# Optimization experiments

Measured on AMD Instinct MI355X. Metric: run time of the kernel, lower is better.

Reference implementation:

```python
import jax, jax.numpy as jnp
import numpy as np

B, T, W, D = 4, 1000, 32, 200
ED, N, DCONV, DTR = 400, 16, 4, 13  # d_inner=2*d_model, d_state, d_conv, dt_rank=ceil(200/16)


def _causal_conv(x, w, b):
    # x: (B, L, ED), depthwise causal conv, kernel DCONV
    L = x.shape[1]
    xp = jnp.pad(x, ((0, 0), (DCONV - 1, 0), (0, 0)))
    y = sum(xp[:, k:k + L, :] * w[:, k] for k in range(DCONV))
    return y + b


def _ssm(x, A_log, Dp, xproj, dtw, dtb):
    # selective scan; x: (B, L, ED)
    A = -jnp.exp(A_log)                      # (ED, N)
    dbc = x @ xproj                          # (B, L, DTR+2N)
    delta, Bm, Cm = dbc[..., :DTR], dbc[..., DTR:DTR + N], dbc[..., DTR + N:]
    dt = jax.nn.softplus(delta @ dtw + dtb)  # (B, L, ED)
    dA = jnp.exp(dt[..., None] * A)                         # (B, L, ED, N)
    dBx = dt[..., None] * Bm[:, :, None, :] * x[..., None]  # (B, L, ED, N)

    def step(h, t):
        dA_t, dBx_t, C_t = t
        h = dA_t * h + dBx_t
        y = jnp.einsum('ben,bn->be', h, C_t)
        return h, y

    h0 = jnp.zeros((x.shape[0], ED, N), x.dtype)
    xs = (dA.transpose(1, 0, 2, 3), dBx.transpose(1, 0, 2, 3), Cm.transpose(1, 0, 2))
    _, ys = jax.lax.scan(step, h0, xs)
    return ys.transpose(1, 0, 2) + Dp * x


def _branch(x, in_proj, conv_w, conv_b, xproj, dtw, dtb, A_log, Dp):
    xz = x @ in_proj
    xp, z = xz[..., :ED], xz[..., ED:]
    xp = jax.nn.silu(_causal_conv(xp, conv_w, conv_b))
    y = _ssm(xp, A_log, Dp, xproj, dtw, dtb)
    return y * jax.nn.silu(z)


def setup_inputs() -> dict:
    key = jax.random.key(0)
    ks = jax.random.split(key, 24)
    s = 0.02
    nrm = lambda k, shape: jax.random.normal(k, shape, jnp.float32) * s
    inp = {}
    inp['input_ids'] = jax.random.normal(ks[0], (B, T, W, D), jnp.float32)
    inp['n_tweets'] = jax.random.randint(ks[1], (B,), 1, T + 1)
    inp['n_words'] = jax.random.randint(ks[2], (B, T), 1, W + 1)
    inp['cls_token'] = jnp.zeros((1, 1, D), jnp.float32)
    inp['w_attn'] = nrm(ks[3], (D, 1))
    inp['b_attn'] = jnp.zeros((1,), jnp.float32)
    inp['norm_w'] = jnp.ones((D,), jnp.float32)
    for i, d in enumerate(('f', 'b')):
        o = i * 8
        inp[f'in_proj_{d}'] = nrm(ks[4 + o], (D, 2 * ED))
        inp[f'conv_w_{d}'] = nrm(ks[5 + o], (ED, DCONV))
        inp[f'conv_b_{d}'] = jnp.zeros((ED,), jnp.float32)
        inp[f'xproj_{d}'] = nrm(ks[6 + o], (ED, DTR + 2 * N))
        inp[f'dtw_{d}'] = nrm(ks[7 + o], (DTR, ED))
        inp[f'dtb_{d}'] = jnp.zeros((ED,), jnp.float32)
        inp[f'A_log_{d}'] = jnp.log(jnp.broadcast_to(jnp.arange(1, N + 1, dtype=jnp.float32), (ED, N)))
        inp[f'D_{d}'] = jnp.ones((ED,), jnp.float32)
    inp['out_proj'] = nrm(ks[20], (ED, D))
    inp['head_w'] = nrm(ks[21], (D, 1))
    inp['head_b'] = jnp.zeros((1,), jnp.float32)
    return inp


def reference(input_ids, n_tweets, n_words, cls_token, w_attn, b_attn, norm_w,
              in_proj_f, conv_w_f, conv_b_f, xproj_f, dtw_f, dtb_f, A_log_f, D_f,
              in_proj_b, conv_w_b, conv_b_b, xproj_b, dtw_b, dtb_b, A_log_b, D_b,
              out_proj, head_w, head_b):
    Bz, Tz, Wz, Dz = input_ids.shape
    # ragged per-tweet attention pooling, fully vectorized with masks
    scores = jnp.squeeze(input_ids @ w_attn, -1) + b_attn[0]        # (B, T, W)
    wmask = jnp.arange(Wz) < n_words[..., None]                     # (B, T, W)
    scores = jnp.where(wmask, scores, -jnp.inf)
    attn = jax.nn.softmax(scores, axis=-1)
    tw = jnp.einsum('btw,btwd->btd', attn, input_ids)               # (B, T, D)
    tmask = jnp.arange(Tz) < n_tweets[:, None]
    tw = jnp.where(tmask[..., None], tw, 0.0)                       # padded tweets stay zero
    pos = Tz // 2
    x = jnp.concatenate([tw[:, :pos], jnp.broadcast_to(cls_token, (Bz, 1, Dz)), tw[:, pos:]], axis=1)
    # one bidirectional Mamba layer: pre-RMSNorm residual block
    xn = x * jax.lax.rsqrt(jnp.mean(x * x, axis=-1, keepdims=True) + 1e-5) * norm_w
    y_f = _branch(xn, in_proj_f, conv_w_f, conv_b_f, xproj_f, dtw_f, dtb_f, A_log_f, D_f)
    y_b = jnp.flip(_branch(jnp.flip(xn, 1), in_proj_b, conv_w_b, conv_b_b, xproj_b, dtw_b, dtb_b, A_log_b, D_b), 1)
    x = x + (y_f + y_b) @ out_proj
    logit = jnp.squeeze(x[:, pos] @ head_w, -1) + head_b[0]
    return jax.nn.sigmoid(logit)
```

## Files before the change

kernel.cpp:

```cpp
#include <hip/hip_runtime.h>
#include <cmath>

#define Bz 4
#define Tz 1000
#define Wz 32
#define Dz 200
#define EDz 400
#define Nz 16
#define DTRz 13
#define Lz 1001
#define POSz 500
#define LPz 501
#define TSTR 512
#define ESP 10
#define NEG_BIG -1e30f

__device__ __forceinline__ float wave_sum(float v) {
#pragma unroll
  for (int o = 32; o; o >>= 1) v += __shfl_xor(v, o);
  return v;
}

__global__ __launch_bounds__(256) void k_front(
    const float* __restrict__ x, const int* __restrict__ n_tweets,
    const int* __restrict__ n_words, const float* __restrict__ w_attn,
    const float* __restrict__ b_attn, const float* __restrict__ norm_w,
    const float* __restrict__ cls, const float* __restrict__ out_proj,
    const float* __restrict__ head_w, const float* __restrict__ ipf,
    const float* __restrict__ ipb, float* __restrict__ xn,
    float* __restrict__ zbuf, float* __restrict__ vbuf) {
  int bid = blockIdx.x;
  int tid = threadIdx.x;
  int wave = tid >> 6, lane = tid & 63;
  if (bid < 9) {
    if (bid == 0) {
      __shared__ float hw[Dz];
      if (tid < Dz) hw[tid] = head_w[tid];
      __syncthreads();
      for (int e = tid; e < EDz; e += 256) {
        float acc = 0.f;
        for (int d = 0; d < Dz; d += 4) {
          float4 ov = *(const float4*)(out_proj + e * Dz + d);
          acc += ov.x * hw[d] + ov.y * hw[d + 1] + ov.z * hw[d + 2] + ov.w * hw[d + 3];
        }
        vbuf[e] = acc;
      }
      return;
    }
    int id = bid - 1;
    int br = id >> 2, b = id & 3;
    __shared__ float xs[Dz];
    __shared__ float s_red[4];
    float val = (tid < Dz) ? cls[tid] : 0.f;
    float sq = wave_sum(val * val);
    if ((tid & 63) == 0) s_red[tid >> 6] = sq;
    __syncthreads();
    float tot = s_red[0] + s_red[1] + s_red[2] + s_red[3];
    float scale = rsqrtf(tot * (1.f / Dz) + 1e-5f);
    if (tid < Dz) {
      float o = val * scale * norm_w[tid];
      xs[tid] = o;
      if (br == 0) xn[((size_t)b * Lz + POSz) * Dz + tid] = o;
    }
    __syncthreads();
    const float* ip = br ? ipb : ipf;
    for (int e = tid; e < EDz; e += 256) {
      float acc = 0.f;
      for (int d = 0; d < Dz; ++d) acc += xs[d] * ip[d * (2 * EDz) + EDz + e];
      zbuf[((size_t)br * Bz + b) * EDz + e] = acc;
    }
    return;
  }
  int bt = (bid - 9) * 4 + wave;
  int b = bt / Tz, t = bt - b * Tz;
  int l = (t < POSz) ? t : t + 1;
  float* outr = xn + ((size_t)b * Lz + l) * Dz;
  int ntw = n_tweets[b]; if (ntw > Tz) ntw = Tz;
  if (t >= ntw) {
    if (lane < 50) *(float4*)(outr + lane * 4) = make_float4(0.f, 0.f, 0.f, 0.f);
    return;
  }
  int nw = n_words[b * Tz + t]; if (nw > Wz) nw = Wz; if (nw < 1) nw = 1;
  const float* xs = x + ((size_t)(b * Tz + t)) * (Wz * Dz);
  int h = lane & 1, w = lane >> 1;
  float sc = 0.f;
  if (w < nw) {
    const float* xr = xs + w * Dz + h * 100;
    const float* wr = w_attn + h * 100;
#pragma unroll
    for (int i = 0; i < 25; ++i) {
      float4 xv = *(const float4*)(xr + i * 4);
      float4 wv = *(const float4*)(wr + i * 4);
      sc += xv.x * wv.x + xv.y * wv.y + xv.z * wv.z + xv.w * wv.w;
    }
  }
  sc += __shfl_xor(sc, 1);
  float scv = (w < nw) ? (sc + b_attn[0]) : NEG_BIG;
  float m = scv;
#pragma unroll
  for (int o = 32; o; o >>= 1) m = fmaxf(m, __shfl_xor(m, o));
  float en = __expf(scv - m);
  float es = (h == 0) ? en : 0.f;
  float tot = wave_sum(es);
  en /= tot;
  float4 val = make_float4(0.f, 0.f, 0.f, 0.f);
  const float* xc = xs + lane * 4;
  for (int ww = 0; ww < nw; ++ww) {
    float aw = __shfl(en, 2 * ww);
    if (lane < 50) {
      float4 xv = *(const float4*)(xc + ww * Dz);
      val.x += aw * xv.x; val.y += aw * xv.y;
      val.z += aw * xv.z; val.w += aw * xv.w;
    }
  }
  float sq = (lane < 50) ? (val.x * val.x + val.y * val.y + val.z * val.z + val.w * val.w) : 0.f;
  sq = wave_sum(sq);
  float scale = rsqrtf(sq * (1.f / Dz) + 1e-5f);
  if (lane < 50) {
    float4 nw4 = *(const float4*)(norm_w + lane * 4);
    float4 o = make_float4(val.x * scale * nw4.x, val.y * scale * nw4.y,
                           val.z * scale * nw4.z, val.w * scale * nw4.w);
    *(float4*)(outr + lane * 4) = o;
  }
}

__global__ __launch_bounds__(256) void k_gemm(
    const float* __restrict__ xn, const float* __restrict__ ipf,
    const float* __restrict__ ipb, float* __restrict__ P) {
  int bid = blockIdx.x;
  int brb = bid / 56;
  int rr = bid - brb * 56;
  int tt = rr / 7, ee = rr - tt * 7;
  int br = brb >> 2, b = brb & 3;
  int t0 = tt * 64, e0 = ee * 64;
  const float* ip = br ? ipb : ipf;
  int tid = threadIdx.x;
  int tx = tid & 15, ty = tid >> 4;

  __shared__ float Xs[16][64 + 4];
  __shared__ float Ws[16][64 + 4];

  float acc[4][4];
#pragma unroll
  for (int i = 0; i < 4; ++i)
#pragma unroll
    for (int j = 0; j < 4; ++j) acc[i][j] = 0.f;

  int xr = tid >> 2, xc = (tid & 3) * 4;
  int wr = tid >> 4, wc = (tid & 15) * 4;
  int t = t0 + xr;
  bool tok = (t < LPz);
  int l = br ? (Lz - 1 - t) : t;
  const float* xrow = xn + ((size_t)b * Lz + l) * Dz;

  for (int dk = 0; dk < 200; dk += 16) {
    float xv[4], wv[4];
#pragma unroll
    for (int c = 0; c < 4; ++c) {
      int d = dk + xc + c;
      xv[c] = (tok && d < Dz) ? xrow[d] : 0.f;
    }
    int dw = dk + wr;
#pragma unroll
    for (int c = 0; c < 4; ++c) {
      int e = e0 + wc + c;
      wv[c] = (dw < Dz && e < EDz) ? ip[(size_t)dw * (2 * EDz) + e] : 0.f;
    }
    __syncthreads();
#pragma unroll
    for (int c = 0; c < 4; ++c) Xs[xc + c][xr] = xv[c];
#pragma unroll
    for (int c = 0; c < 4; ++c) Ws[wr][wc + c] = wv[c];
    __syncthreads();
#pragma unroll
    for (int k = 0; k < 16; ++k) {
      float4 a4 = *(const float4*)&Xs[k][ty * 4];
      float4 b4 = *(const float4*)&Ws[k][tx * 4];
      float av[4] = {a4.x, a4.y, a4.z, a4.w};
      float bv[4] = {b4.x, b4.y, b4.z, b4.w};
#pragma unroll
      for (int i = 0; i < 4; ++i)
#pragma unroll
        for (int j = 0; j < 4; ++j) acc[i][j] += av[i] * bv[j];
    }
  }
#pragma unroll
  for (int j = 0; j < 4; ++j) {
    int e = e0 + tx * 4 + j;
    if (e < EDz) {
      float4 o = make_float4(acc[0][j], acc[1][j], acc[2][j], acc[3][j]);
      *(float4*)&P[((size_t)brb * EDz + e) * TSTR + t0 + ty * 4] = o;
    }
  }
}

__global__ __launch_bounds__(256) void k_mid(
    const float* __restrict__ P,
    const float* __restrict__ cwf, const float* __restrict__ cwb,
    const float* __restrict__ cbf, const float* __restrict__ cbb,
    const float* __restrict__ xpjf, const float* __restrict__ xpjb,
    float* __restrict__ xp_t, float* __restrict__ dbcp) {
  int bid = blockIdx.x;
  int esp = bid % ESP;
  int rem = bid / ESP;
  int tc = rem & 7, brb = rem >> 3;
  int br = brb >> 2;
  int tid = threadIdx.x;
  int wave = tid >> 6, lane = tid & 63;
  int t = tc * 64 + lane;
  const float* cw = br ? cwb : cwf;
  const float* cb = br ? cbb : cbf;
  const float* xpj = br ? xpjb : xpjf;

  __shared__ float sred[4][64][45];

  float accq[45];
#pragma unroll
  for (int q = 0; q < 45; ++q) accq[q] = 0.f;

  const float* Pb = P + (size_t)brb * EDz * TSTR;
  int e0 = esp * 40 + wave * 10;
#pragma unroll 2
  for (int i = 0; i < 10; ++i) {
    int e = e0 + i;
    const float* pr = Pb + (size_t)e * TSTR;
    float p0 = (t >= 3) ? pr[t - 3] : 0.f;
    float p1 = (t >= 2) ? pr[t - 2] : 0.f;
    float p2 = (t >= 1) ? pr[t - 1] : 0.f;
    float p3 = pr[t];
    float4 c4 = *(const float4*)(cw + e * 4);
    float a = cb[e] + c4.x * p0 + c4.y * p1 + c4.z * p2 + c4.w * p3;
    float sp = a / (1.f + __expf(-a));
    xp_t[((size_t)brb * EDz + e) * TSTR + t] = sp;
    const float* xq = xpj + e * 45;
#pragma unroll
    for (int q = 0; q < 45; ++q) accq[q] += sp * xq[q];
  }
#pragma unroll
  for (int q = 0; q < 45; ++q) sred[wave][lane][q] = accq[q];
  __syncthreads();
  if (wave < 2) {
#pragma unroll
    for (int q = 0; q < 45; ++q)
      sred[wave][lane][q] += sred[wave + 2][lane][q];
  }
  __syncthreads();
  if (wave == 0) {
    float* dp = dbcp + ((size_t)(esp * 8 + brb) * 45) * TSTR + t;
#pragma unroll
    for (int q = 0; q < 45; ++q)
      dp[(size_t)q * TSTR] = sred[0][lane][q] + sred[1][lane][q];
  }
}

__global__ __launch_bounds__(256) void k_dt2(
    const float* __restrict__ dbcp,
    const float* __restrict__ dtwf, const float* __restrict__ dtwb,
    const float* __restrict__ dtbf, const float* __restrict__ dtbb,
    float* __restrict__ dt_t, float* __restrict__ Bm_t,
    float* __restrict__ Cend) {
  int bid = blockIdx.x;
  int egrp = bid % 11;
  int rem = bid / 11;
  int tc = rem & 7, brb = rem >> 3;
  int br = brb >> 2;
  int tid = threadIdx.x;
  int wave = tid >> 6, lane = tid & 63;
  int t = tc * 64 + lane;
  const size_t espstr = (size_t)8 * 45 * TSTR;

  if (egrp == 10) {
    for (int idx = tid; idx < 16 * 64; idx += 256) {
      int n = idx >> 6, tl = idx & 63;
      size_t base = ((size_t)brb * 45 + 13 + n) * TSTR + tc * 64 + tl;
      float s = 0.f;
#pragma unroll
      for (int esp = 0; esp < ESP; ++esp) s += dbcp[base + esp * espstr];
      Bm_t[((size_t)brb * Nz + n) * TSTR + tc * 64 + tl] = s;
    }
    if (tc == 7 && tid < Nz) {
      size_t base = ((size_t)brb * 45 + 29 + tid) * TSTR + POSz;
      float s = 0.f;
#pragma unroll
      for (int esp = 0; esp < ESP; ++esp) s += dbcp[base + esp * espstr];
      Cend[brb * Nz + tid] = s;
    }
    return;
  }

  __shared__ float dfin[DTRz][64];
  for (int idx = tid; idx < DTRz * 64; idx += 256) {
    int q = idx >> 6, tl = idx & 63;
    size_t base = ((size_t)brb * 45 + q) * TSTR + tc * 64 + tl;
    float s = 0.f;
#pragma unroll
    for (int esp = 0; esp < ESP; ++esp) s += dbcp[base + esp * espstr];
    dfin[q][tl] = s;
  }
  __syncthreads();
  const float* dtw = br ? dtwb : dtwf;
  const float* dtb = br ? dtbb : dtbf;
  float dq[DTRz];
#pragma unroll
  for (int q = 0; q < DTRz; ++q) dq[q] = dfin[q][lane];
  int e0 = egrp * 40 + wave * 10;
#pragma unroll 2
  for (int i = 0; i < 10; ++i) {
    int e = e0 + i;
    float s = dtb[e];
#pragma unroll
    for (int q = 0; q < DTRz; ++q) s += dq[q] * dtw[q * EDz + e];
    float dtv = (s > 20.f) ? s : log1pf(__expf(s));
    dt_t[((size_t)brb * EDz + e) * TSTR + t] = dtv;
  }
}

__global__ __launch_bounds__(64) void k_scan(
    const float* __restrict__ xp_t, const float* __restrict__ dt_t,
    const float* __restrict__ Bm_t, const float* __restrict__ Cend,
    const float* __restrict__ Alogf, const float* __restrict__ Alogb,
    const float* __restrict__ Dpf, const float* __restrict__ Dpb,
    const float* __restrict__ zbuf, const float* __restrict__ vbuf,
    float* __restrict__ ybuf) {
  int blk = blockIdx.x;
  int br = blk / (Bz * EDz);
  int rem = blk - br * (Bz * EDz);
  int b = rem / EDz, e = rem - b * EDz;
  int lane = threadIdx.x;
  const float* A_log = br ? Alogb : Alogf;
  const float* Dp = br ? Dpb : Dpf;
  float A[Nz];
  {
    const float4* ap = (const float4*)(A_log + e * Nz);
#pragma unroll
    for (int q = 0; q < 4; ++q) {
      float4 a4 = ap[q];
      A[q * 4 + 0] = -__expf(a4.x); A[q * 4 + 1] = -__expf(a4.y);
      A[q * 4 + 2] = -__expf(a4.z); A[q * 4 + 3] = -__expf(a4.w);
    }
  }
  size_t base = ((size_t)(br * Bz + b) * EDz + e) * TSTR;
  const float* dtp = dt_t + base;
  const float* xpp = xp_t + base;
  const float* bmp = Bm_t + (size_t)(br * Bz + b) * Nz * TSTR;
  float loc = 0.f;
#pragma unroll
  for (int c = 0; c < 8; ++c) {
    int t = c * 64 + lane;
    if (t < LPz) loc += dtp[t];
  }
  float Stot = wave_sum(loc);
  float acc[Nz];
#pragma unroll
  for (int n = 0; n < Nz; ++n) acc[n] = 0.f;
  float carry = 0.f;
  for (int c = 0; c < 8; ++c) {
    int t = c * 64 + lane;
    bool act = t < LPz;
    float dtt = 0.f, xv = 0.f;
    if (act) { dtt = dtp[t]; xv = xpp[t]; }
    float s = dtt;
#pragma unroll
    for (int o = 1; o < 64; o <<= 1) {
      float u = __shfl_up(s, o);
      s += (lane >= o) ? u : 0.f;
    }
    float S = carry + s;
    carry += __shfl(s, 63);
    float wt = dtt * xv;
    float decay = Stot - S;
#pragma unroll
    for (int n = 0; n < Nz; ++n) {
      float bv = 0.f;
      if (act) bv = bmp[n * TSTR + t];
      acc[n] += __expf(A[n] * decay) * wt * bv;
    }
  }
#pragma unroll
  for (int o = 32; o; o >>= 1) {
#pragma unroll
    for (int n = 0; n < Nz; ++n) acc[n] += __shfl_xor(acc[n], o);
  }
  if (lane == 0) {
    float y = Dp[e] * xpp[LPz - 1];
#pragma unroll
    for (int n = 0; n < Nz; ++n) y += Cend[(br * Bz + b) * Nz + n] * acc[n];
    float zz = zbuf[((size_t)br * Bz + b) * EDz + e];
    float sz = zz / (1.f + __expf(-zz));
    ybuf[((size_t)br * Bz + b) * EDz + e] = y * sz * vbuf[e];
  }
}

__global__ __launch_bounds__(256) void k_final(
    const float* __restrict__ cls, const float* __restrict__ head_w,
    const float* __restrict__ head_b, const float* __restrict__ ybuf,
    float* __restrict__ out) {
  int tid = threadIdx.x;
  int b = tid >> 6, lane = tid & 63;
  float acc = 0.f;
  for (int e = lane; e < EDz; e += 64)
    acc += ybuf[(size_t)b * EDz + e] + ybuf[(size_t)(Bz + b) * EDz + e];
  for (int d = lane; d < Dz; d += 64) acc += cls[d] * head_w[d];
  acc = wave_sum(acc);
  if (lane == 0) out[b] = 1.f / (1.f + __expf(-(acc + head_b[0])));
}

extern "C" void kernel_launch(void* const* d_in, const int* in_sizes, int n_in,
                              void* d_out, int out_size, void* d_ws, size_t ws_size,
                              hipStream_t stream) {
  const float* input_ids = (const float*)d_in[0];
  const int* n_tweets = (const int*)d_in[1];
  const int* n_words = (const int*)d_in[2];
  const float* cls = (const float*)d_in[3];
  const float* w_attn = (const float*)d_in[4];
  const float* b_attn = (const float*)d_in[5];
  const float* norm_w = (const float*)d_in[6];
  const float* ip[2] = {(const float*)d_in[7], (const float*)d_in[15]};
  const float* cw[2] = {(const float*)d_in[8], (const float*)d_in[16]};
  const float* cb[2] = {(const float*)d_in[9], (const float*)d_in[17]};
  const float* xpj[2] = {(const float*)d_in[10], (const float*)d_in[18]};
  const float* dtw[2] = {(const float*)d_in[11], (const float*)d_in[19]};
  const float* dtbp[2] = {(const float*)d_in[12], (const float*)d_in[20]};
  const float* Alog[2] = {(const float*)d_in[13], (const float*)d_in[21]};
  const float* Dpp[2] = {(const float*)d_in[14], (const float*)d_in[22]};
  const float* out_proj = (const float*)d_in[23];
  const float* head_w = (const float*)d_in[24];
  const float* head_b = (const float*)d_in[25];
  float* out = (float*)d_out;

  float* ws = (float*)d_ws;
  float* xn = ws;
  float* Pbuf = xn + 800800;
  float* xp_t = Pbuf + 1638400;
  float* dt_t = xp_t + 1638400;
  float* Bm_t = dt_t + 1638400;
  float* dbcp = Bm_t + 65536;
  float* Cend = dbcp + 1843200;
  float* zbuf = Cend + 128;
  float* vbuf = zbuf + 3200;
  float* ybuf = vbuf + 400;

  hipLaunchKernelGGL(k_front, dim3(9 + Bz * Tz / 4), dim3(256), 0, stream,
                     input_ids, n_tweets, n_words, w_attn, b_attn, norm_w,
                     cls, out_proj, head_w, ip[0], ip[1], xn, zbuf, vbuf);
  hipLaunchKernelGGL(k_gemm, dim3(2 * Bz * 8 * 7), dim3(256), 0, stream,
                     xn, ip[0], ip[1], Pbuf);
  hipLaunchKernelGGL(k_mid, dim3(2 * Bz * 8 * ESP), dim3(256), 0, stream,
                     Pbuf, cw[0], cw[1], cb[0], cb[1], xpj[0], xpj[1],
                     xp_t, dbcp);
  hipLaunchKernelGGL(k_dt2, dim3(2 * Bz * 8 * 11), dim3(256), 0, stream,
                     dbcp, dtw[0], dtw[1], dtbp[0], dtbp[1],
                     dt_t, Bm_t, Cend);
  hipLaunchKernelGGL(k_scan, dim3(2 * Bz * EDz), dim3(64), 0, stream,
                     xp_t, dt_t, Bm_t, Cend, Alog[0], Alog[1], Dpp[0], Dpp[1],
                     zbuf, vbuf, ybuf);
  hipLaunchKernelGGL(k_final, dim3(1), dim3(256), 0, stream,
                     cls, head_w, head_b, ybuf, out);
}
```

Before: 107.4 us.

## Fuse in-proj GEMM, causal conv, x-proj and dt-proj into one kernel

Replaces the separate GEMM, conv+x-proj, and dt/reduction kernels with a single k_heavy kernel. Each block handles a 16-token chunk (with a 3-token halo) across all 400 channels, keeping the projection output, the conv/SiLU result and the 45-wide dbc values in shared memory. This removes the global P and dbcp intermediates, the split-E partial-sum reduction and two launches. In exchange the grid shrinks to 256 blocks of 512 threads with heavy shared-memory use, and the halo rows of the in-proj GEMM are recomputed per chunk.

```diff
diff --git a/kernel.cpp b/kernel.cpp
--- a/kernel.cpp
+++ b/kernel.cpp
@@ -12,7 +12,7 @@
 #define POSz 500
 #define LPz 501
 #define TSTR 512
-#define ESP 10
+#define TCH 16
 #define NEG_BIG -1e30f
 
 __device__ __forceinline__ float wave_sum(float v) {
@@ -124,194 +124,168 @@
   }
 }
 
-__global__ __launch_bounds__(256) void k_gemm(
-    const float* __restrict__ xn, const float* __restrict__ ipf,
-    const float* __restrict__ ipb, float* __restrict__ P) {
-  int bid = blockIdx.x;
-  int brb = bid / 56;
-  int rr = bid - brb * 56;
-  int tt = rr / 7, ee = rr - tt * 7;
-  int br = brb >> 2, b = brb & 3;
-  int t0 = tt * 64, e0 = ee * 64;
-  const float* ip = br ? ipb : ipf;
-  int tid = threadIdx.x;
-  int tx = tid & 15, ty = tid >> 4;
-
-  __shared__ float Xs[16][64 + 4];
-  __shared__ float Ws[16][64 + 4];
-
-  float acc[4][4];
-#pragma unroll
-  for (int i = 0; i < 4; ++i)
-#pragma unroll
-    for (int j = 0; j < 4; ++j) acc[i][j] = 0.f;
-
-  int xr = tid >> 2, xc = (tid & 3) * 4;
-  int wr = tid >> 4, wc = (tid & 15) * 4;
-  int t = t0 + xr;
-  bool tok = (t < LPz);
-  int l = br ? (Lz - 1 - t) : t;
-  const float* xrow = xn + ((size_t)b * Lz + l) * Dz;
-
-  for (int dk = 0; dk < 200; dk += 16) {
-    float xv[4], wv[4];
-#pragma unroll
-    for (int c = 0; c < 4; ++c) {
-      int d = dk + xc + c;
-      xv[c] = (tok && d < Dz) ? xrow[d] : 0.f;
-    }
-    int dw = dk + wr;
-#pragma unroll
-    for (int c = 0; c < 4; ++c) {
-      int e = e0 + wc + c;
-      wv[c] = (dw < Dz && e < EDz) ? ip[(size_t)dw * (2 * EDz) + e] : 0.f;
-    }
-    __syncthreads();
-#pragma unroll
-    for (int c = 0; c < 4; ++c) Xs[xc + c][xr] = xv[c];
-#pragma unroll
-    for (int c = 0; c < 4; ++c) Ws[wr][wc + c] = wv[c];
-    __syncthreads();
-#pragma unroll
-    for (int k = 0; k < 16; ++k) {
-      float4 a4 = *(const float4*)&Xs[k][ty * 4];
-      float4 b4 = *(const float4*)&Ws[k][tx * 4];
-      float av[4] = {a4.x, a4.y, a4.z, a4.w};
-      float bv[4] = {b4.x, b4.y, b4.z, b4.w};
-#pragma unroll
-      for (int i = 0; i < 4; ++i)
-#pragma unroll
-        for (int j = 0; j < 4; ++j) acc[i][j] += av[i] * bv[j];
-    }
-  }
-#pragma unroll
-  for (int j = 0; j < 4; ++j) {
-    int e = e0 + tx * 4 + j;
-    if (e < EDz) {
-      float4 o = make_float4(acc[0][j], acc[1][j], acc[2][j], acc[3][j]);
-      *(float4*)&P[((size_t)brb * EDz + e) * TSTR + t0 + ty * 4] = o;
-    }
-  }
-}
-
-__global__ __launch_bounds__(256) void k_mid(
-    const float* __restrict__ P,
+__global__ __launch_bounds__(512) void k_heavy(
+    const float* __restrict__ xn,
+    const float* __restrict__ ipf, const float* __restrict__ ipb,
     const float* __restrict__ cwf, const float* __restrict__ cwb,
     const float* __restrict__ cbf, const float* __restrict__ cbb,
     const float* __restrict__ xpjf, const float* __restrict__ xpjb,
-    float* __restrict__ xp_t, float* __restrict__ dbcp) {
+    const float* __restrict__ dtwf, const float* __restrict__ dtwb,
+    const float* __restrict__ dtbf, const float* __restrict__ dtbb,
+    float* __restrict__ xp_t, float* __restrict__ dt_t,
+    float* __restrict__ Bm_t, float* __restrict__ Cend) {
   int bid = blockIdx.x;
-  int esp = bid % ESP;
-  int rem = bid / ESP;
-  int tc = rem & 7, brb = rem >> 3;
-  int br = brb >> 2;
+  int tc = bid & 31, brb = bid >> 5;
+  int br = brb >> 2, b = brb & 3;
+  int t0 = tc * TCH;
   int tid = threadIdx.x;
   int wave = tid >> 6, lane = tid & 63;
-  int t = tc * 64 + lane;
+  const float* ip = br ? ipb : ipf;
   const float* cw = br ? cwb : cwf;
   const float* cb = br ? cbb : cbf;
   const float* xpj = br ? xpjb : xpjf;
-
-  __shared__ float sred[4][64][45];
-
-  float accq[45];
-#pragma unroll
-  for (int q = 0; q < 45; ++q) accq[q] = 0.f;
-
-  const float* Pb = P + (size_t)brb * EDz * TSTR;
-  int e0 = esp * 40 + wave * 10;
-#pragma unroll 2
-  for (int i = 0; i < 10; ++i) {
-    int e = e0 + i;
-    const float* pr = Pb + (size_t)e * TSTR;
-    float p0 = (t >= 3) ? pr[t - 3] : 0.f;
-    float p1 = (t >= 2) ? pr[t - 2] : 0.f;
-    float p2 = (t >= 1) ? pr[t - 1] : 0.f;
-    float p3 = pr[t];
-    float4 c4 = *(const float4*)(cw + e * 4);
-    float a = cb[e] + c4.x * p0 + c4.y * p1 + c4.z * p2 + c4.w * p3;
-    float sp = a / (1.f + __expf(-a));
-    xp_t[((size_t)brb * EDz + e) * TSTR + t] = sp;
-    const float* xq = xpj + e * 45;
-#pragma unroll
-    for (int q = 0; q < 45; ++q) accq[q] += sp * xq[q];
-  }
-#pragma unroll
-  for (int q = 0; q < 45; ++q) sred[wave][lane][q] = accq[q];
-  __syncthreads();
-  if (wave < 2) {
-#pragma unroll
-    for (int q = 0; q < 45; ++q)
-      sred[wave][lane][q] += sred[wave + 2][lane][q];
-  }
-  __syncthreads();
-  if (wave == 0) {
-    float* dp = dbcp + ((size_t)(esp * 8 + brb) * 45) * TSTR + t;
-#pragma unroll
-    for (int q = 0; q < 45; ++q)
-      dp[(size_t)q * TSTR] = sred[0][lane][q] + sred[1][lane][q];
-  }
-}
-
-__global__ __launch_bounds__(256) void k_dt2(
-    const float* __restrict__ dbcp,
-    const float* __restrict__ dtwf, const float* __restrict__ dtwb,
-    const float* __restrict__ dtbf, const float* __restrict__ dtbb,
-    float* __restrict__ dt_t, float* __restrict__ Bm_t,
-    float* __restrict__ Cend) {
-  int bid = blockIdx.x;
-  int egrp = bid % 11;
-  int rem = bid / 11;
-  int tc = rem & 7, brb = rem >> 3;
-  int br = brb >> 2;
-  int tid = threadIdx.x;
-  int wave = tid >> 6, lane = tid & 63;
-  int t = tc * 64 + lane;
-  const size_t espstr = (size_t)8 * 45 * TSTR;
-
-  if (egrp == 10) {
-    for (int idx = tid; idx < 16 * 64; idx += 256) {
-      int n = idx >> 6, tl = idx & 63;
-      size_t base = ((size_t)brb * 45 + 13 + n) * TSTR + tc * 64 + tl;
-      float s = 0.f;
-#pragma unroll
-      for (int esp = 0; esp < ESP; ++esp) s += dbcp[base + esp * espstr];
-      Bm_t[((size_t)brb * Nz + n) * TSTR + tc * 64 + tl] = s;
-    }
-    if (tc == 7 && tid < Nz) {
-      size_t base = ((size_t)brb * 45 + 29 + tid) * TSTR + POSz;
-      float s = 0.f;
-#pragma unroll
-      for (int esp = 0; esp < ESP; ++esp) s += dbcp[base + esp * espstr];
-      Cend[brb * Nz + tid] = s;
-    }
-    return;
-  }
-
-  __shared__ float dfin[DTRz][64];
-  for (int idx = tid; idx < DTRz * 64; idx += 256) {
-    int q = idx >> 6, tl = idx & 63;
-    size_t base = ((size_t)brb * 45 + q) * TSTR + tc * 64 + tl;
-    float s = 0.f;
-#pragma unroll
-    for (int esp = 0; esp < ESP; ++esp) s += dbcp[base + esp * espstr];
-    dfin[q][tl] = s;
-  }
-  __syncthreads();
   const float* dtw = br ? dtwb : dtwf;
   const float* dtb = br ? dtbb : dtbf;
-  float dq[DTRz];
-#pragma unroll
-  for (int q = 0; q < DTRz; ++q) dq[q] = dfin[q][lane];
-  int e0 = egrp * 40 + wave * 10;
-#pragma unroll 2
-  for (int i = 0; i < 10; ++i) {
-    int e = e0 + i;
-    float s = dtb[e];
-#pragma unroll
-    for (int q = 0; q < DTRz; ++q) s += dq[q] * dtw[q * EDz + e];
-    float dtv = (s > 20.f) ? s : log1pf(__expf(s));
-    dt_t[((size_t)brb * EDz + e) * TSTR + t] = dtv;
+
+  __shared__ float WsBuf[16 * 400];
+  __shared__ float Xs[16][20];
+  __shared__ float Pb[20][404];
+  __shared__ float dbc[45][17];
+
+  int tx = tid % 100, ty = tid / 100;
+  float acc[4][4];
+#pragma unroll
+  for (int i = 0; i < 4; ++i)
+#pragma unroll
+    for (int j = 0; j < 4; ++j) acc[i][j] = 0.f;
+
+  for (int dk = 0; dk < 200; dk += 16) {
+    if (tid < 320) {
+      int r = tid >> 4, k = tid & 15;
+      int t = t0 - 3 + r;
+      float v = 0.f;
+      if (t >= 0 && t < LPz) {
+        int l = br ? (Lz - 1 - t) : t;
+        v = xn[((size_t)b * Lz + l) * Dz + dk + k];
+      }
+      Xs[k][r] = v;
+    }
+    for (int i = tid; i < 1600; i += 512) {
+      int k = i / 100, c4 = i - k * 100;
+      float4 wv = *(const float4*)(ip + (size_t)(dk + k) * (2 * EDz) + c4 * 4);
+      *(float4*)&WsBuf[k * 400 + c4 * 4] = wv;
+    }
+    __syncthreads();
+    if (ty < 5) {
+#pragma unroll
+      for (int k = 0; k < 16; ++k) {
+        float4 a4 = *(const float4*)&Xs[k][ty * 4];
+        float4 b4 = *(const float4*)&WsBuf[k * 400 + tx * 4];
+        float av[4] = {a4.x, a4.y, a4.z, a4.w};
+        float bv[4] = {b4.x, b4.y, b4.z, b4.w};
+#pragma unroll
+        for (int i = 0; i < 4; ++i)
+#pragma unroll
+          for (int j = 0; j < 4; ++j) acc[i][j] += av[i] * bv[j];
+      }
+    }
+    __syncthreads();
+  }
+  if (ty < 5) {
+#pragma unroll
+    for (int i = 0; i < 4; ++i)
+      *(float4*)&Pb[ty * 4 + i][tx * 4] =
+          make_float4(acc[i][0], acc[i][1], acc[i][2], acc[i][3]);
+  }
+  __syncthreads();
+
+  if (tid < EDz) {
+    int e = tid;
+    float4 c4 = *(const float4*)(cw + e * 4);
+    float cbe = cb[e];
+    float p0 = Pb[0][e], p1 = Pb[1][e], p2 = Pb[2][e];
+    float xv[TCH];
+#pragma unroll
+    for (int i = 0; i < TCH; ++i) {
+      float p3 = Pb[i + 3][e];
+      float a = cbe + c4.x * p0 + c4.y * p1 + c4.z * p2 + c4.w * p3;
+      float sp = a / (1.f + __expf(-a));
+      xv[i] = sp;
+      Pb[i][e] = sp;
+      p0 = p1; p1 = p2; p2 = p3;
+    }
+    float* xpp = xp_t + ((size_t)brb * EDz + e) * TSTR + t0;
+    *(float4*)(xpp) = make_float4(xv[0], xv[1], xv[2], xv[3]);
+    *(float4*)(xpp + 4) = make_float4(xv[4], xv[5], xv[6], xv[7]);
+    *(float4*)(xpp + 8) = make_float4(xv[8], xv[9], xv[10], xv[11]);
+    *(float4*)(xpp + 12) = make_float4(xv[12], xv[13], xv[14], xv[15]);
+  }
+  __syncthreads();
+
+  {
+    int tl = lane & 15, s = lane >> 4;
+    int q0 = s * 12;
+    float accq[12];
+#pragma unroll
+    for (int qq = 0; qq < 12; ++qq) accq[qq] = 0.f;
+    int e_lo = wave * 50;
+    for (int i = 0; i < 50; ++i) {
+      int e = e_lo + i;
+      float sp = Pb[tl][e];
+      const float* xq = xpj + e * 45 + q0;
+#pragma unroll
+      for (int qq = 0; qq < 12; ++qq) {
+        float xv = (q0 + qq < 45) ? xq[qq] : 0.f;
+        accq[qq] += sp * xv;
+      }
+    }
+    float* sred = WsBuf;
+#pragma unroll
+    for (int qq = 0; qq < 12; ++qq) {
+      if (q0 + qq < 45) sred[((size_t)wave * 16 + tl) * 45 + q0 + qq] = accq[qq];
+    }
+  }
+  __syncthreads();
+  {
+    const float* sred = WsBuf;
+    for (int idx = tid; idx < 45 * 16; idx += 512) {
+      int t = idx / 45, q = idx - (idx / 45) * 45;
+      float ssum = 0.f;
+#pragma unroll
+      for (int w = 0; w < 8; ++w) ssum += sred[((size_t)w * 16 + t) * 45 + q];
+      dbc[q][t] = ssum;
+    }
+  }
+  __syncthreads();
+
+  if (tid < EDz) {
+    int e = tid;
+    float wq[DTRz];
+#pragma unroll
+    for (int q = 0; q < DTRz; ++q) wq[q] = dtw[q * EDz + e];
+    float dtbe = dtb[e];
+    float dv[TCH];
+#pragma unroll
+    for (int i = 0; i < TCH; ++i) {
+      float s = dtbe;
+#pragma unroll
+      for (int q = 0; q < DTRz; ++q) s += dbc[q][i] * wq[q];
+      dv[i] = (s > 20.f) ? s : log1pf(__expf(s));
+    }
+    float* dtp = dt_t + ((size_t)brb * EDz + e) * TSTR + t0;
+    *(float4*)(dtp) = make_float4(dv[0], dv[1], dv[2], dv[3]);
+    *(float4*)(dtp + 4) = make_float4(dv[4], dv[5], dv[6], dv[7]);
+    *(float4*)(dtp + 8) = make_float4(dv[8], dv[9], dv[10], dv[11]);
+    *(float4*)(dtp + 12) = make_float4(dv[12], dv[13], dv[14], dv[15]);
+  } else if (tid >= 448) {
+    int q2 = tid - 448;
+    int n = q2 >> 2, j = q2 & 3;
+    float4 o = make_float4(dbc[13 + n][j * 4], dbc[13 + n][j * 4 + 1],
+                           dbc[13 + n][j * 4 + 2], dbc[13 + n][j * 4 + 3]);
+    *(float4*)&Bm_t[((size_t)brb * Nz + n) * TSTR + t0 + j * 4] = o;
+  } else if (tc == 31 && tid >= 416 && tid < 432) {
+    int n = tid - 416;
+    Cend[brb * Nz + n] = dbc[29 + n][POSz - 496];
   }
 }
 
@@ -371,8 +345,7 @@
     float decay = Stot - S;
 #pragma unroll
     for (int n = 0; n < Nz; ++n) {
-      float bv = 0.f;
-      if (act) bv = bmp[n * TSTR + t];
+      float bv = act ? bmp[n * TSTR + t] : 0.f;
       acc[n] += __expf(A[n] * decay) * wt * bv;
     }
   }
@@ -430,12 +403,10 @@
 
   float* ws = (float*)d_ws;
   float* xn = ws;
-  float* Pbuf = xn + 800800;
-  float* xp_t = Pbuf + 1638400;
+  float* xp_t = xn + 800800;
   float* dt_t = xp_t + 1638400;
   float* Bm_t = dt_t + 1638400;
-  float* dbcp = Bm_t + 65536;
-  float* Cend = dbcp + 1843200;
+  float* Cend = Bm_t + 65536;
   float* zbuf = Cend + 128;
   float* vbuf = zbuf + 3200;
   float* ybuf = vbuf + 400;
@@ -443,14 +414,10 @@
   hipLaunchKernelGGL(k_front, dim3(9 + Bz * Tz / 4), dim3(256), 0, stream,
                      input_ids, n_tweets, n_words, w_attn, b_attn, norm_w,
                      cls, out_proj, head_w, ip[0], ip[1], xn, zbuf, vbuf);
-  hipLaunchKernelGGL(k_gemm, dim3(2 * Bz * 8 * 7), dim3(256), 0, stream,
-                     xn, ip[0], ip[1], Pbuf);
-  hipLaunchKernelGGL(k_mid, dim3(2 * Bz * 8 * ESP), dim3(256), 0, stream,
-                     Pbuf, cw[0], cw[1], cb[0], cb[1], xpj[0], xpj[1],
-                     xp_t, dbcp);
-  hipLaunchKernelGGL(k_dt2, dim3(2 * Bz * 8 * 11), dim3(256), 0, stream,
-                     dbcp, dtw[0], dtw[1], dtbp[0], dtbp[1],
-                     dt_t, Bm_t, Cend);
+  hipLaunchKernelGGL(k_heavy, dim3(2 * Bz * 32), dim3(512), 0, stream,
+                     xn, ip[0], ip[1], cw[0], cw[1], cb[0], cb[1],
+                     xpj[0], xpj[1], dtw[0], dtw[1], dtbp[0], dtbp[1],
+                     xp_t, dt_t, Bm_t, Cend);
   hipLaunchKernelGGL(k_scan, dim3(2 * Bz * EDz), dim3(64), 0, stream,
                      xp_t, dt_t, Bm_t, Cend, Alog[0], Alog[1], Dpp[0], Dpp[1],
                      zbuf, vbuf, ybuf);
```

After: 110.9 us. 3.3% more time.
